# Optimization experiments

Hardware: AMD Instinct MI355X
Metric: run time of the kernel (lower is better)

## Reference

```python
import jax, jax.numpy as jnp
import numpy as np

NUM_CAPS = 10       # J: output capsules
PREV_NODES = 16384  # P: input capsules (16*32*32)
IN_CH = 8           # D: input capsule dim
OUT_CH = 16         # O: output capsule dim
BATCH = 32
ROUTING_ITERS = 3


def squash(s):
    # s: (..., O). v = (|s|^2 / (1+|s|^2)) * s / |s|
    sq = jnp.sum(s * s, axis=-1, keepdims=True)
    return s * (sq / ((1.0 + sq) * jnp.sqrt(sq)))


def setup_inputs() -> dict:
    key = jax.random.key(0)
    kx, kw = jax.random.split(key)
    x = jax.random.normal(kx, (BATCH, PREV_NODES, IN_CH), dtype=jnp.float32)
    W = jax.random.normal(kw, (NUM_CAPS, PREV_NODES, IN_CH, OUT_CH), dtype=jnp.float32)
    return {"x": x, "W": W}


def reference(x, W):
    # u_hat[b,j,p,:] = x[b,p,:] @ W[j,p,:,:]  -> (B, J, P, O)
    u_hat = jnp.einsum('bpd,jpdo->bjpo', x, W)
    temp_u_hat = jax.lax.stop_gradient(u_hat)
    B = x.shape[0]
    b = jnp.zeros((B, NUM_CAPS, PREV_NODES, 1), dtype=u_hat.dtype)
    for _ in range(ROUTING_ITERS - 1):
        c = jax.nn.softmax(b, axis=1)                   # over output capsules
        s = jnp.sum(c * temp_u_hat, axis=2)             # (B, J, O)
        v = squash(s)
        uv = jnp.einsum('bjpo,bjo->bjp', temp_u_hat, v)[..., None]
        b = b + uv
    c = jax.nn.softmax(b, axis=1)
    s = jnp.sum(c * u_hat, axis=2)
    v = squash(s)                                       # (B, J, O)
    return v
```

## Files before the change

### kernel.cpp

```cpp
#include <hip/hip_runtime.h>

typedef _Float16 half_t;
typedef half_t h2 __attribute__((ext_vector_type(2)));

#define J 10
#define P 16384
#define D 8
#define O 16
#define B 32

#define PTILE 16
#define NB ((P / PTILE) * 2)
#define SJO (B * J * O)

#define WT_PLS 2576
#define WT_PLH (WT_PLS / 2)
#define XS_OFF (PTILE * WT_PLS)
#define SMEM_BYTES (XS_OFF + PTILE * 16 * 16)

template <int CTRL>
__device__ __forceinline__ float dpp_mov_f(float v) {
    return __int_as_float(__builtin_amdgcn_update_dpp(
        0, __float_as_int(v), CTRL, 0xF, 0xF, true));
}
__device__ __forceinline__ float row_sum16(float v) {
    v += dpp_mov_f<0xB1>(v);
    v += dpp_mov_f<0x4E>(v);
    v += dpp_mov_f<0x124>(v);
    v += dpp_mov_f<0x128>(v);
    return v;
}

__device__ __forceinline__ h2 pkrtz(float a, float b) {
    return __builtin_bit_cast(h2, __builtin_amdgcn_cvt_pkrtz(a, b));
}

union U4H { uint4 u; h2 h[4]; };
union U1H { unsigned u; h2 h; };

__global__ __launch_bounds__(256, 3) void caps_pass(
    const float* __restrict__ x, const float* __restrict__ W,
    const unsigned* __restrict__ vs16, float* __restrict__ s_acc, int first)
{
    __shared__ char smem[SMEM_BYTES];
    half_t* Wt = (half_t*)smem;
    half_t* xs = (half_t*)(smem + XS_OFF);
    float* s_blk = (float*)smem;

    const int tid = threadIdx.x;
    const int i = blockIdx.x;
    const int bg = (i >> 3) & 1;
    const int pt = (i & 7) | ((i >> 4) << 3);
    const int p0 = pt * PTILE;

#pragma unroll
    for (int k = 0; k < 2; ++k) {
        const int idx = k * 256 + tid;
        const int o4 = idx & 3, d = (idx >> 2) & 7, pl = idx >> 5;
        const float* src = W + (size_t)p0 * (D * O) + (size_t)idx * 4;
        half_t* dst = Wt + pl * WT_PLH + (o4 * 4) * 8 + d;
        for (int j = 0; j < J; ++j) {
            float4 f = *(const float4*)(src + (size_t)j * P * (D * O));
            half_t* dj = dst + j * 128;
            dj[0]  = (half_t)f.x;
            dj[8]  = (half_t)f.y;
            dj[16] = (half_t)f.z;
            dj[24] = (half_t)f.w;
        }
    }
    {
        const int bl = tid >> 4, pl = tid & 15;
        const float4* xp = (const float4*)(x + ((size_t)(bg * 16 + bl) * P + p0 + pl) * D);
        float4 a = xp[0], c = xp[1];
        U4H pk;
        pk.h[0] = pkrtz(a.x, a.y);
        pk.h[1] = pkrtz(a.z, a.w);
        pk.h[2] = pkrtz(c.x, c.y);
        pk.h[3] = pkrtz(c.z, c.w);
        *(uint4*)(xs + (size_t)(pl * 16 + bl) * 8) = pk.u;
    }

    const int o = tid & 15, bsub = (tid >> 4) & 3, wid = tid >> 6;

    h2 vsp[4][5];
    if (!first) {
#pragma unroll
        for (int bc = 0; bc < 4; ++bc) {
            const int b = bg * 16 + bc * 4 + bsub;
            const unsigned* src = vs16 + ((size_t)b * 16 + o) * 8;
            U4H q4; q4.u = *(const uint4*)src;
            U1H q1; q1.u = src[4];
            vsp[bc][0] = q4.h[0]; vsp[bc][1] = q4.h[1];
            vsp[bc][2] = q4.h[2]; vsp[bc][3] = q4.h[3];
            vsp[bc][4] = q1.h;
        }
    }
    __syncthreads();

    float acc[4][J];
#pragma unroll
    for (int bc = 0; bc < 4; ++bc)
#pragma unroll
        for (int j = 0; j < J; ++j) acc[bc][j] = 0.f;

#pragma unroll 1
    for (int pi = 0; pi < 4; ++pi) {
        const int pl = wid * 4 + pi;

        U4H xf[4];
#pragma unroll
        for (int bc = 0; bc < 4; ++bc)
            xf[bc].u = *(const uint4*)(xs + (size_t)(pl * 16 + bc * 4 + bsub) * 8);

        h2 uh_pk[2][J];
#pragma unroll
        for (int jh = 0; jh < 2; ++jh) {
            U4H wv[5];
#pragma unroll
            for (int j5 = 0; j5 < 5; ++j5)
                wv[j5].u = *(const uint4*)(Wt + (size_t)pl * WT_PLH
                                           + ((jh * 5 + j5) * 16 + o) * 8);
#pragma unroll
            for (int j5 = 0; j5 < 5; ++j5) {
                const int j = jh * 5 + j5;
                float u[4];
#pragma unroll
                for (int bc = 0; bc < 4; ++bc) {
                    float s = 0.f;
#pragma unroll
                    for (int dq = 0; dq < 4; ++dq)
                        s = __builtin_amdgcn_fdot2(wv[j5].h[dq], xf[bc].h[dq], s, false);
                    u[bc] = s;
                }
                if (first) {
#pragma unroll
                    for (int bc = 0; bc < 4; ++bc)
                        acc[bc][j] = fmaf(0.1f, u[bc], acc[bc][j]);
                } else {
                    uh_pk[0][j] = pkrtz(u[0], u[1]);
                    uh_pk[1][j] = pkrtz(u[2], u[3]);
                }
            }
        }

        if (!first) {
#pragma unroll
            for (int bc = 0; bc < 4; ++bc) {
                float uhf[J], lg[J];
#pragma unroll
                for (int j = 0; j < J; ++j) {
                    uhf[j] = (float)uh_pk[bc >> 1][j][bc & 1];
                    lg[j] = row_sum16(uhf[j] * (float)vsp[bc][j >> 1][j & 1]);
                }
                float e[J], Z = 0.f;
#pragma unroll
                for (int j = 0; j < J; ++j) { e[j] = __expf(lg[j]); Z += e[j]; }
                const float rZ = __builtin_amdgcn_rcpf(Z);
#pragma unroll
                for (int j = 0; j < J; ++j)
                    acc[bc][j] = fmaf(e[j] * rZ, uhf[j], acc[bc][j]);
            }
        }
    }

    __syncthreads();
#pragma unroll
    for (int bc = 0; bc < 4; ++bc) {
        const int bl = bc * 4 + bsub;
#pragma unroll
        for (int j = 0; j < J; ++j)
            s_blk[(wid * 16 + bl) * 164 + j * 16 + o] = acc[bc][j];
    }
    __syncthreads();
    for (int t = tid; t < 16 * 160; t += 256) {
        const int bl = t / 160, r = t - bl * 160;
        const float v = s_blk[bl * 164 + r] + s_blk[(16 + bl) * 164 + r]
                      + s_blk[(32 + bl) * 164 + r] + s_blk[(48 + bl) * 164 + r];
        atomicAdd(&s_acc[(bg * 16 + bl) * 160 + r], v);
    }
}

__global__ __launch_bounds__(256) void caps_squash(
    float* __restrict__ s_acc, float* __restrict__ Vsum,
    unsigned* __restrict__ vs16, float* __restrict__ out, int write_out)
{
    const int b = blockIdx.x;
    const int o = threadIdx.x & 15;
    const int j = threadIdx.x >> 4;
    const bool act = j < J;
    const int idx = (b * J + (act ? j : 0)) * O + o;
    float s = act ? s_acc[idx] : 0.f;
    const float sq = row_sum16(s * s);
    float vnew = 0.f;
    if (act) {
        const float scale = sqrtf(sq) / (1.f + sq);
        const float v = s * scale;
        vnew = Vsum[idx] + v;
        Vsum[idx] = vnew;
        s_acc[idx] = 0.f;
        if (write_out) out[idx] = v;
    }
    const float vpart = __shfl_xor(vnew, 16, 64);
    if (act && !(j & 1)) {
        U1H t; t.h = pkrtz(vnew, vpart);
        vs16[((size_t)b * 16 + o) * 8 + (j >> 1)] = t.u;
    }
}

__global__ __launch_bounds__(256) void caps_zero(float* __restrict__ ws)
{
    const int i = blockIdx.x * 256 + threadIdx.x;
    if (i < 2 * SJO) ws[i] = 0.f;
}

extern "C" void kernel_launch(void* const* d_in, const int* in_sizes, int n_in,
                              void* d_out, int out_size, void* d_ws, size_t ws_size,
                              hipStream_t stream)
{
    const float* x = (const float*)d_in[0];
    const float* W = (const float*)d_in[1];
    float* out = (float*)d_out;

    float* s_acc = (float*)d_ws;
    float* Vsum  = s_acc + SJO;
    unsigned* vs16 = (unsigned*)(Vsum + SJO);

    caps_zero<<<dim3(40), 256, 0, stream>>>(s_acc);

    for (int it = 0; it < 3; ++it) {
        caps_pass<<<dim3(NB), 256, 0, stream>>>(x, W, vs16, s_acc, it == 0 ? 1 : 0);
        caps_squash<<<dim3(B), 256, 0, stream>>>(s_acc, Vsum, vs16, out, it == 2 ? 1 : 0);
    }
}
```

Measured before the change: 266.1 us.

## Compute u_hat with MFMA 16x16x16 and cover all batches per block

The per-lane fdot2 dot products are replaced with mfma_f32_16x16x16f16 instructions. The K dimension is padded from 8 to 16 by masking half of the x fragment to zero. Each block now covers all 32 batches with 512 threads, so W is loaded and converted once per p-tile instead of twice. The routing logits are reduced with ds_swizzle and bpermute to match the MFMA output layout, and the v cache layout changes to suit. The cost is half-wasted MFMA work from the zero padding, plus two extra reduction rounds with more syncs.

```diff
diff --git a/kernel.cpp b/kernel.cpp
--- a/kernel.cpp
+++ b/kernel.cpp
@@ -2,6 +2,8 @@
 
 typedef _Float16 half_t;
 typedef half_t h2 __attribute__((ext_vector_type(2)));
+typedef half_t h4 __attribute__((ext_vector_type(4)));
+typedef float f4 __attribute__((ext_vector_type(4)));
 
 #define J 10
 #define P 16384
@@ -10,13 +12,13 @@
 #define B 32
 
 #define PTILE 16
-#define NB ((P / PTILE) * 2)
+#define NB (P / PTILE)
 #define SJO (B * J * O)
 
 #define WT_PLS 2576
 #define WT_PLH (WT_PLS / 2)
 #define XS_OFF (PTILE * WT_PLS)
-#define SMEM_BYTES (XS_OFF + PTILE * 16 * 16)
+#define SMEM_BYTES (XS_OFF + PTILE * B * 16)
 
 template <int CTRL>
 __device__ __forceinline__ float dpp_mov_f(float v) {
@@ -35,12 +37,22 @@
     return __builtin_bit_cast(h2, __builtin_amdgcn_cvt_pkrtz(a, b));
 }
 
+__device__ __forceinline__ float xor16_add(float v) {
+    int s = __builtin_amdgcn_ds_swizzle(__float_as_int(v), 0x401F);
+    return v + __int_as_float(s);
+}
+__device__ __forceinline__ float xor32_add(float v, int bpa) {
+    int s = __builtin_amdgcn_ds_bpermute(bpa, __float_as_int(v));
+    return v + __int_as_float(s);
+}
+
 union U4H { uint4 u; h2 h[4]; };
+union U2H { uint2 u2; h2 h[2]; h4 v; };
 union U1H { unsigned u; h2 h; };
 
-__global__ __launch_bounds__(256, 3) void caps_pass(
+__global__ __launch_bounds__(512, 4) void caps_pass(
     const float* __restrict__ x, const float* __restrict__ W,
-    const unsigned* __restrict__ vs16, float* __restrict__ s_acc, int first)
+    const unsigned* __restrict__ vh, float* __restrict__ s_acc, int first)
 {
     __shared__ char smem[SMEM_BYTES];
     half_t* Wt = (half_t*)smem;
@@ -48,17 +60,13 @@
     float* s_blk = (float*)smem;
 
     const int tid = threadIdx.x;
-    const int i = blockIdx.x;
-    const int bg = (i >> 3) & 1;
-    const int pt = (i & 7) | ((i >> 4) << 3);
-    const int p0 = pt * PTILE;
-
-#pragma unroll
-    for (int k = 0; k < 2; ++k) {
-        const int idx = k * 256 + tid;
-        const int o4 = idx & 3, d = (idx >> 2) & 7, pl = idx >> 5;
-        const float* src = W + (size_t)p0 * (D * O) + (size_t)idx * 4;
+    const int p0 = blockIdx.x * PTILE;
+
+    {
+        const int o4 = tid & 3, d = (tid >> 2) & 7, pl = tid >> 5;
+        const float* src = W + (size_t)p0 * (D * O) + (size_t)tid * 4;
         half_t* dst = Wt + pl * WT_PLH + (o4 * 4) * 8 + d;
+#pragma unroll
         for (int j = 0; j < J; ++j) {
             float4 f = *(const float4*)(src + (size_t)j * P * (D * O));
             half_t* dj = dst + j * 128;
@@ -70,119 +78,114 @@
     }
     {
         const int bl = tid >> 4, pl = tid & 15;
-        const float4* xp = (const float4*)(x + ((size_t)(bg * 16 + bl) * P + p0 + pl) * D);
+        const float4* xp = (const float4*)(x + ((size_t)bl * P + p0 + pl) * D);
         float4 a = xp[0], c = xp[1];
         U4H pk;
         pk.h[0] = pkrtz(a.x, a.y);
         pk.h[1] = pkrtz(a.z, a.w);
         pk.h[2] = pkrtz(c.x, c.y);
         pk.h[3] = pkrtz(c.z, c.w);
-        *(uint4*)(xs + (size_t)(pl * 16 + bl) * 8) = pk.u;
-    }
-
-    const int o = tid & 15, bsub = (tid >> 4) & 3, wid = tid >> 6;
-
-    h2 vsp[4][5];
+        *(uint4*)(xs + (size_t)(pl * 32 + bl) * 8) = pk.u;
+    }
+
+    const int lane = tid & 63;
+    const int wv   = tid >> 6;
+    const int bh   = wv >> 2;
+    const int wid2 = wv & 3;
+    const int bl16 = lane & 15;
+    const int q    = lane >> 4;
+    const unsigned kmask = (q < 2) ? 0xFFFFFFFFu : 0u;
+    const int bpa = ((lane ^ 32) & 63) << 2;
+
+    U2H vf[J];
     if (!first) {
-#pragma unroll
-        for (int bc = 0; bc < 4; ++bc) {
-            const int b = bg * 16 + bc * 4 + bsub;
-            const unsigned* src = vs16 + ((size_t)b * 16 + o) * 8;
-            U4H q4; q4.u = *(const uint4*)src;
-            U1H q1; q1.u = src[4];
-            vsp[bc][0] = q4.h[0]; vsp[bc][1] = q4.h[1];
-            vsp[bc][2] = q4.h[2]; vsp[bc][3] = q4.h[3];
-            vsp[bc][4] = q1.h;
-        }
+        const unsigned* vp = vh + (size_t)(bh * 16 + bl16) * J * 8 + 2 * q;
+#pragma unroll
+        for (int j = 0; j < J; ++j)
+            vf[j].u2 = *(const uint2*)(vp + j * 8);
     }
     __syncthreads();
 
-    float acc[4][J];
-#pragma unroll
-    for (int bc = 0; bc < 4; ++bc)
-#pragma unroll
-        for (int j = 0; j < J; ++j) acc[bc][j] = 0.f;
+    f4 acc[J];
+#pragma unroll
+    for (int j = 0; j < J; ++j) acc[j] = (f4){0.f, 0.f, 0.f, 0.f};
+    const f4 zf = (f4){0.f, 0.f, 0.f, 0.f};
 
 #pragma unroll 1
     for (int pi = 0; pi < 4; ++pi) {
-        const int pl = wid * 4 + pi;
-
-        U4H xf[4];
-#pragma unroll
-        for (int bc = 0; bc < 4; ++bc)
-            xf[bc].u = *(const uint4*)(xs + (size_t)(pl * 16 + bc * 4 + bsub) * 8);
-
-        h2 uh_pk[2][J];
-#pragma unroll
-        for (int jh = 0; jh < 2; ++jh) {
-            U4H wv[5];
-#pragma unroll
-            for (int j5 = 0; j5 < 5; ++j5)
-                wv[j5].u = *(const uint4*)(Wt + (size_t)pl * WT_PLH
-                                           + ((jh * 5 + j5) * 16 + o) * 8);
-#pragma unroll
-            for (int j5 = 0; j5 < 5; ++j5) {
-                const int j = jh * 5 + j5;
-                float u[4];
-#pragma unroll
-                for (int bc = 0; bc < 4; ++bc) {
-                    float s = 0.f;
-#pragma unroll
-                    for (int dq = 0; dq < 4; ++dq)
-                        s = __builtin_amdgcn_fdot2(wv[j5].h[dq], xf[bc].h[dq], s, false);
-                    u[bc] = s;
-                }
-                if (first) {
-#pragma unroll
-                    for (int bc = 0; bc < 4; ++bc)
-                        acc[bc][j] = fmaf(0.1f, u[bc], acc[bc][j]);
-                } else {
-                    uh_pk[0][j] = pkrtz(u[0], u[1]);
-                    uh_pk[1][j] = pkrtz(u[2], u[3]);
-                }
+        const int pl = wid2 * 4 + pi;
+
+        U2H xv;
+        xv.u2 = *(const uint2*)(xs + (size_t)(pl * 32 + bh * 16 + bl16) * 8
+                                + 4 * (q & 1));
+        xv.u2.x &= kmask;
+        xv.u2.y &= kmask;
+        const h4 bfrag = xv.v;
+
+        const half_t* wbase = Wt + pl * WT_PLH + bl16 * 8 + 4 * (q & 1);
+
+        h2 uh[J][2];
+        float lg[J];
+#pragma unroll
+        for (int j = 0; j < J; ++j) {
+            const h4 af = *(const h4*)(wbase + j * 128);
+            f4 u = __builtin_amdgcn_mfma_f32_16x16x16f16(af, bfrag, zf, 0, 0, 0);
+            if (first) {
+#pragma unroll
+                for (int r = 0; r < 4; ++r)
+                    acc[j][r] = fmaf(0.1f, u[r], acc[j][r]);
+            } else {
+                uh[j][0] = pkrtz(u[0], u[1]);
+                uh[j][1] = pkrtz(u[2], u[3]);
+                lg[j] = __builtin_amdgcn_fdot2(uh[j][1], vf[j].h[1],
+                        __builtin_amdgcn_fdot2(uh[j][0], vf[j].h[0], 0.f, false),
+                        false);
             }
         }
 
         if (!first) {
 #pragma unroll
-            for (int bc = 0; bc < 4; ++bc) {
-                float uhf[J], lg[J];
-#pragma unroll
-                for (int j = 0; j < J; ++j) {
-                    uhf[j] = (float)uh_pk[bc >> 1][j][bc & 1];
-                    lg[j] = row_sum16(uhf[j] * (float)vsp[bc][j >> 1][j & 1]);
-                }
-                float e[J], Z = 0.f;
-#pragma unroll
-                for (int j = 0; j < J; ++j) { e[j] = __expf(lg[j]); Z += e[j]; }
-                const float rZ = __builtin_amdgcn_rcpf(Z);
-#pragma unroll
-                for (int j = 0; j < J; ++j)
-                    acc[bc][j] = fmaf(e[j] * rZ, uhf[j], acc[bc][j]);
+            for (int j = 0; j < J; ++j) lg[j] = xor16_add(lg[j]);
+#pragma unroll
+            for (int j = 0; j < J; ++j) lg[j] = xor32_add(lg[j], bpa);
+            float e[J], Z = 0.f;
+#pragma unroll
+            for (int j = 0; j < J; ++j) { e[j] = __expf(lg[j]); Z += e[j]; }
+            const float rZ = __builtin_amdgcn_rcpf(Z);
+#pragma unroll
+            for (int j = 0; j < J; ++j) {
+                const float c = e[j] * rZ;
+                acc[j][0] = fmaf(c, (float)uh[j][0][0], acc[j][0]);
+                acc[j][1] = fmaf(c, (float)uh[j][0][1], acc[j][1]);
+                acc[j][2] = fmaf(c, (float)uh[j][1][0], acc[j][2]);
+                acc[j][3] = fmaf(c, (float)uh[j][1][1], acc[j][3]);
             }
         }
     }
 
     __syncthreads();
-#pragma unroll
-    for (int bc = 0; bc < 4; ++bc) {
-        const int bl = bc * 4 + bsub;
-#pragma unroll
-        for (int j = 0; j < J; ++j)
-            s_blk[(wid * 16 + bl) * 164 + j * 16 + o] = acc[bc][j];
-    }
-    __syncthreads();
-    for (int t = tid; t < 16 * 160; t += 256) {
-        const int bl = t / 160, r = t - bl * 160;
-        const float v = s_blk[bl * 164 + r] + s_blk[(16 + bl) * 164 + r]
-                      + s_blk[(32 + bl) * 164 + r] + s_blk[(48 + bl) * 164 + r];
-        atomicAdd(&s_acc[(bg * 16 + bl) * 160 + r], v);
+#pragma unroll 1
+    for (int r = 0; r < 2; ++r) {
+        if (bh == r) {
+#pragma unroll
+            for (int j = 0; j < J; ++j)
+                *(f4*)&s_blk[(size_t)(wid2 * 16 + bl16) * 164 + j * 16 + 4 * q]
+                    = acc[j];
+        }
+        __syncthreads();
+        for (int t = tid; t < 16 * 160; t += 512) {
+            const int bl = t / 160, rr = t - bl * 160;
+            const float v = s_blk[bl * 164 + rr] + s_blk[(16 + bl) * 164 + rr]
+                          + s_blk[(32 + bl) * 164 + rr] + s_blk[(48 + bl) * 164 + rr];
+            atomicAdd(&s_acc[(size_t)(r * 16 + bl) * 160 + rr], v);
+        }
+        __syncthreads();
     }
 }
 
 __global__ __launch_bounds__(256) void caps_squash(
     float* __restrict__ s_acc, float* __restrict__ Vsum,
-    unsigned* __restrict__ vs16, float* __restrict__ out, int write_out)
+    unsigned* __restrict__ vh, float* __restrict__ out, int write_out)
 {
     const int b = blockIdx.x;
     const int o = threadIdx.x & 15;
@@ -200,10 +203,10 @@
         s_acc[idx] = 0.f;
         if (write_out) out[idx] = v;
     }
-    const float vpart = __shfl_xor(vnew, 16, 64);
-    if (act && !(j & 1)) {
+    const float vpart = __shfl_xor(vnew, 1, 64);
+    if (act && !(o & 1)) {
         U1H t; t.h = pkrtz(vnew, vpart);
-        vs16[((size_t)b * 16 + o) * 8 + (j >> 1)] = t.u;
+        vh[(size_t)(b * J + j) * 8 + (o >> 1)] = t.u;
     }
 }
 
@@ -223,12 +226,12 @@
 
     float* s_acc = (float*)d_ws;
     float* Vsum  = s_acc + SJO;
-    unsigned* vs16 = (unsigned*)(Vsum + SJO);
+    unsigned* vh = (unsigned*)(Vsum + SJO);
 
     caps_zero<<<dim3(40), 256, 0, stream>>>(s_acc);
 
     for (int it = 0; it < 3; ++it) {
-        caps_pass<<<dim3(NB), 256, 0, stream>>>(x, W, vs16, s_acc, it == 0 ? 1 : 0);
-        caps_squash<<<dim3(B), 256, 0, stream>>>(s_acc, Vsum, vs16, out, it == 2 ? 1 : 0);
-    }
-}
+        caps_pass<<<dim3(NB), 512, 0, stream>>>(x, W, vh, s_acc, it == 0 ? 1 : 0);
+        caps_squash<<<dim3(B), 256, 0, stream>>>(s_acc, Vsum, vh, out, it == 2 ? 1 : 0);
+    }
+}
```

Measured after the change: 283.4 us. 1.07x slower.
